# Optimization experiments

Hardware: AMD Instinct MI355X
Metric: run time of the kernel (lower is better)

Reference implementation:

```python
import jax, jax.numpy as jnp
import numpy as np

MAX_ITERS = 10


def setup_inputs() -> dict:
    key = jax.random.key(0)
    k1, k2, k3, k4, k5 = jax.random.split(key, 5)
    B, D, H = 8192, 2048, 2048
    s = 1.0 / np.sqrt(H)  # torch default init scale (uniform); we use scaled normal
    return {
        "encoded": jax.random.normal(k1, (B, D), dtype=jnp.float32),
        "w_ih": jax.random.normal(k2, (3 * H, D), dtype=jnp.float32) * s,
        "w_hh": jax.random.normal(k3, (3 * H, H), dtype=jnp.float32) * s,
        "b_ih": jax.random.normal(k4, (3 * H,), dtype=jnp.float32) * s,
        "b_hh": jax.random.normal(k5, (3 * H,), dtype=jnp.float32) * s,
    }


def reference(encoded, w_ih, w_hh, b_ih, b_hh):
    """Iterative GRUCell recurrence (training-mode: full max_iters, no early exit).

    PyTorch GRUCell math:
      r = sigmoid(W_ir x + b_ir + W_hr h + b_hr)
      z = sigmoid(W_iz x + b_iz + W_hz h + b_hz)
      n = tanh(W_in x + b_in + r * (W_hn h + b_hn))
      h' = (1 - z) * n + z * h
    """
    H = w_hh.shape[1]
    # Input projection is constant across iterations (gru_input never changes).
    gi = encoded @ w_ih.T + b_ih  # [B, 3H]
    gi_r, gi_z, gi_n = gi[:, :H], gi[:, H:2 * H], gi[:, 2 * H:]

    def step(h, _):
        gh = h @ w_hh.T + b_hh  # [B, 3H]
        gh_r, gh_z, gh_n = gh[:, :H], gh[:, H:2 * H], gh[:, 2 * H:]
        r = jax.nn.sigmoid(gi_r + gh_r)
        z = jax.nn.sigmoid(gi_z + gh_z)
        n = jnp.tanh(gi_n + r * gh_n)
        h_next = (1.0 - z) * n + z * h
        return h_next, None

    h0 = jnp.zeros((encoded.shape[0], H), dtype=encoded.dtype)
    h, _ = jax.lax.scan(step, h0, None, length=MAX_ITERS)
    return h
```

## Files before the change

kernel.cpp:

```cpp
#include <hip/hip_runtime.h>

typedef _Float16 f16_t;
typedef _Float16 f16x4 __attribute__((ext_vector_type(4)));
typedef _Float16 f16x8 __attribute__((ext_vector_type(8)));
typedef float floatx4 __attribute__((ext_vector_type(4)));

#define GLDS16(gptr, lptr) __builtin_amdgcn_global_load_lds( \
    (const __attribute__((address_space(1))) void*)(gptr),   \
    (__attribute__((address_space(3))) void*)(lptr), 16, 0, 0)

__device__ __forceinline__ float sigmoidf_fast(float x) {
    return 1.f / (1.f + __expf(-x));
}
__device__ __forceinline__ float tanhf_fast(float x) {
    float e = __expf(2.f * x);
    return 1.f - 2.f / (e + 1.f);
}

#define GATE_STRIDE 16777216L

__global__ __launch_bounds__(256)
void cvt_f32_f16(const float* __restrict__ in, f16_t* __restrict__ out, long n)
{
    long i = ((long)blockIdx.x * 256 + threadIdx.x) * 8;
    if (i >= n) return;
    floatx4 a = *(const floatx4*)(in + i);
    floatx4 b = *(const floatx4*)(in + i + 4);
    f16x8 o;
    o[0] = (f16_t)a[0]; o[1] = (f16_t)a[1]; o[2] = (f16_t)a[2]; o[3] = (f16_t)a[3];
    o[4] = (f16_t)b[0]; o[5] = (f16_t)b[1]; o[6] = (f16_t)b[2]; o[7] = (f16_t)b[3];
    *(f16x8*)(out + i) = o;
}

__global__ __launch_bounds__(256, 2)
void gemm_gi(const f16_t* __restrict__ A,
             const f16_t* __restrict__ W,
             const float* __restrict__ bias,
             f16_t* __restrict__ giF)
{
    const int K = 2048;
    __shared__ __align__(16) f16_t As[128 * 32];
    __shared__ __align__(16) f16_t Ws[128 * 32];
    const int tid  = threadIdx.x;
    const int lane = tid & 63;
    const int wave = tid >> 6;
    const int m0 = blockIdx.x * 128;
    const int n0 = blockIdx.y * 128;
    const int wm = (wave >> 1) * 64;
    const int wn = (wave & 1) * 64;

    floatx4 acc[4][4] = {};

    const int srow = lane >> 2;
    const int skc  = (((lane & 3) ^ ((srow >> 1) & 3))) * 8;
    const int fr = lane & 15;
    const int jq = lane >> 4;
    const int jsw = (jq ^ ((fr >> 1) & 3)) * 8;

    for (int k0 = 0; k0 < K; k0 += 32) {
        #pragma unroll
        for (int j = 0; j < 2; ++j) {
            int c = j * 4 + wave;
            int row = c * 16 + srow;
            GLDS16(A + (size_t)(m0 + row) * K + k0 + skc, As + c * 512);
        }
        #pragma unroll
        for (int j = 0; j < 2; ++j) {
            int c = j * 4 + wave;
            int row = c * 16 + srow;
            GLDS16(W + (size_t)(n0 + row) * K + k0 + skc, Ws + c * 512);
        }
        __syncthreads();

        f16x8 a_frag[4], b_frag[4];
        #pragma unroll
        for (int t = 0; t < 4; ++t)
            a_frag[t] = *(const f16x8*)(As + (wm + t * 16 + fr) * 32 + jsw);
        #pragma unroll
        for (int t = 0; t < 4; ++t)
            b_frag[t] = *(const f16x8*)(Ws + (wn + t * 16 + fr) * 32 + jsw);
        #pragma unroll
        for (int tm = 0; tm < 4; ++tm)
            #pragma unroll
            for (int tn = 0; tn < 4; ++tn)
                acc[tm][tn] = __builtin_amdgcn_mfma_f32_16x16x32_f16(
                    a_frag[tm], b_frag[tn], acc[tm][tn], 0, 0, 0);
        __syncthreads();
    }

    const int g   = n0 >> 11;
    const int tNb = ((n0 & 2047) >> 4) + (wn >> 4);
    #pragma unroll
    for (int tm = 0; tm < 4; ++tm) {
        int tM = (m0 + wm + tm * 16) >> 4;
        #pragma unroll
        for (int tn = 0; tn < 4; ++tn) {
            int tN = tNb + tn;
            int n  = n0 + wn + tn * 16 + fr;
            float b = bias[n];
            f16x4 v;
            #pragma unroll
            for (int r = 0; r < 4; ++r) v[r] = (f16_t)(acc[tm][tn][r] + b);
            *(f16x4*)(giF + ((size_t)(g * 512 + tM) * 128 + tN) * 256 + lane * 4) = v;
        }
    }
}

__global__ __launch_bounds__(256)
void gru_init(const f16_t* __restrict__ giF,
              const float* __restrict__ bhh,
              f16_t* __restrict__ h16)
{
    const int H = 2048;
    __shared__ __align__(16) f16_t hp[128 * 72];
    const int tid  = threadIdx.x;
    const int lane = tid & 63;
    const int wave = tid >> 6;
    const int m0 = blockIdx.x * 128;
    const int n0 = blockIdx.y * 64;
    const int wm = (wave >> 1) * 64;
    const int wn = (wave & 1) * 32;
    const int colL = lane & 15;
    const int rq = (lane >> 4) * 4;

    #pragma unroll
    for (int tm = 0; tm < 4; ++tm) {
        int tM = (m0 + wm + tm * 16) >> 4;
        #pragma unroll
        for (int tn = 0; tn < 2; ++tn) {
            int tN = ((n0 + wn) >> 4) + tn;
            size_t base = ((size_t)tM * 128 + tN) * 256 + lane * 4;
            f16x4 g_r = *(const f16x4*)(giF + base);
            f16x4 g_z = *(const f16x4*)(giF + base + GATE_STRIDE);
            f16x4 g_n = *(const f16x4*)(giF + base + 2 * GATE_STRIDE);
            int n = n0 + wn + tn * 16 + colL;
            float br = bhh[n], bz = bhh[H + n], bn = bhh[2 * H + n];
            #pragma unroll
            for (int r = 0; r < 4; ++r) {
                float rr = sigmoidf_fast((float)g_r[r] + br);
                float zz = sigmoidf_fast((float)g_z[r] + bz);
                float nn = tanhf_fast((float)g_n[r] + rr * bn);
                float h = (1.f - zz) * nn;
                hp[(wm + tm * 16 + rq + r) * 72 + wn + tn * 16 + colL] = (f16_t)h;
            }
        }
    }
    __syncthreads();
    #pragma unroll
    for (int i = 0; i < 4; ++i) {
        int r2 = i * 32 + (tid >> 3);
        int ch = tid & 7;
        f16x8 v = *(const f16x8*)(hp + r2 * 72 + ch * 8);
        *(f16x8*)(h16 + (size_t)(m0 + r2) * H + n0 + ch * 8) = v;
    }
}

__global__ __launch_bounds__(256, 2)
void gru_step(const f16_t* __restrict__ Wh,
              const float* __restrict__ bhh,
              const f16_t* __restrict__ giF,
              const f16_t* __restrict__ hin,
              f16_t* __restrict__ hout,
              float* __restrict__ out32)
{
    const int K = 2048, H = 2048;
    __shared__ __align__(16) f16_t smem[128 * 64 + 3 * 64 * 64];
    f16_t* As  = smem;
    f16_t* Wsm = smem + 128 * 64;
    const int tid  = threadIdx.x;
    const int lane = tid & 63;
    const int wave = tid >> 6;

    const int bid   = blockIdx.x;
    const int xcd   = bid & 7;
    const int rblk  = bid >> 3;
    const int m0 = (rblk >> 2) * 128;
    const int n0 = (xcd * 4 + (rblk & 3)) * 64;

    const int wm = (wave >> 1) * 64;
    const int wn = (wave & 1) * 32;

    floatx4 acc[3][4][2] = {};

    const int srow8 = lane >> 3;
    const int sgk   = ((lane & 7) ^ srow8) * 8;
    const int fr = lane & 15;
    const int jq = lane >> 4;
    const int rq = (lane >> 4) * 4;

    f16x4 hold16[4][2];

    for (int k0 = 0; k0 < K; k0 += 64) {
        #pragma unroll
        for (int j = 0; j < 4; ++j) {
            int c = j * 4 + wave;
            int row = c * 8 + srow8;
            GLDS16(hin + (size_t)(m0 + row) * K + k0 + sgk, As + c * 512);
        }
        #pragma unroll
        for (int j = 0; j < 6; ++j) {
            int c = j * 4 + wave;
            int g = c >> 3;
            int cw = c & 7;
            int row = cw * 8 + srow8;
            GLDS16(Wh + (size_t)(g * H + n0 + row) * K + k0 + sgk,
                   Wsm + c * 512);
        }
        __syncthreads();

        if (k0 == n0) {
            #pragma unroll
            for (int tm = 0; tm < 4; ++tm) {
                #pragma unroll
                for (int tn = 0; tn < 2; ++tn) {
                    #pragma unroll
                    for (int r = 0; r < 4; ++r) {
                        int row_a = wm + tm * 16 + rq + r;
                        int kloc  = wn + tn * 16 + fr;
                        int slot  = (kloc >> 3) ^ (row_a & 7);
                        hold16[tm][tn][r] =
                            As[row_a * 64 + slot * 8 + (kloc & 7)];
                    }
                }
            }
        }

        #pragma unroll
        for (int ksub = 0; ksub < 2; ++ksub) {
            f16x8 a_frag[4];
            #pragma unroll
            for (int t = 0; t < 4; ++t) {
                int row = wm + t * 16 + fr;
                int slot = (ksub * 4 + jq) ^ (row & 7);
                a_frag[t] = *(const f16x8*)(As + row * 64 + slot * 8);
            }
            #pragma unroll
            for (int g = 0; g < 3; ++g) {
                #pragma unroll
                for (int tn = 0; tn < 2; ++tn) {
                    int row_w = wn + tn * 16 + fr;
                    int slot = (ksub * 4 + jq) ^ (row_w & 7);
                    f16x8 b_frag = *(const f16x8*)(Wsm + g * 4096 +
                                                   row_w * 64 + slot * 8);
                    #pragma unroll
                    for (int tm = 0; tm < 4; ++tm)
                        acc[g][tm][tn] = __builtin_amdgcn_mfma_f32_16x16x32_f16(
                            a_frag[tm], b_frag, acc[g][tm][tn], 0, 0, 0);
                }
            }
        }
        __syncthreads();
    }

    f16x4 hv[4][2];
    #pragma unroll
    for (int tm = 0; tm < 4; ++tm) {
        int tM = (m0 + wm + tm * 16) >> 4;
        #pragma unroll
        for (int tn = 0; tn < 2; ++tn) {
            int tN = ((n0 + wn) >> 4) + tn;
            size_t base = ((size_t)tM * 128 + tN) * 256 + lane * 4;
            f16x4 g_r = *(const f16x4*)(giF + base);
            f16x4 g_z = *(const f16x4*)(giF + base + GATE_STRIDE);
            f16x4 g_n = *(const f16x4*)(giF + base + 2 * GATE_STRIDE);
            int n = n0 + wn + tn * 16 + fr;
            float br = bhh[n], bz = bhh[H + n], bn = bhh[2 * H + n];
            #pragma unroll
            for (int r = 0; r < 4; ++r) {
                int m = m0 + wm + tm * 16 + rq + r;
                float rr = sigmoidf_fast((float)g_r[r] + acc[0][tm][tn][r] + br);
                float zz = sigmoidf_fast((float)g_z[r] + acc[1][tm][tn][r] + bz);
                float nn = tanhf_fast((float)g_n[r] +
                                      rr * (acc[2][tm][tn][r] + bn));
                float hold = (float)hold16[tm][tn][r];
                float hnew = (1.f - zz) * nn + zz * hold;
                hv[tm][tn][r] = (f16_t)hnew;
                if (out32) out32[(size_t)m * H + n] = hnew;
            }
        }
    }

    if (!out32) {
        f16_t* hp = smem;
        #pragma unroll
        for (int tm = 0; tm < 4; ++tm)
            #pragma unroll
            for (int tn = 0; tn < 2; ++tn)
                #pragma unroll
                for (int r = 0; r < 4; ++r)
                    hp[(wm + tm * 16 + rq + r) * 72 + wn + tn * 16 + fr] =
                        hv[tm][tn][r];
        __syncthreads();
        #pragma unroll
        for (int i = 0; i < 4; ++i) {
            int r2 = i * 32 + (tid >> 3);
            int ch = tid & 7;
            f16x8 v = *(const f16x8*)(hp + r2 * 72 + ch * 8);
            *(f16x8*)(hout + (size_t)(m0 + r2) * H + n0 + ch * 8) = v;
        }
    }
}

extern "C" void kernel_launch(void* const* d_in, const int* in_sizes, int n_in,
                              void* d_out, int out_size, void* d_ws, size_t ws_size,
                              hipStream_t stream) {
    const float* x    = (const float*)d_in[0];
    const float* w_ih = (const float*)d_in[1];
    const float* w_hh = (const float*)d_in[2];
    const float* b_ih = (const float*)d_in[3];
    const float* b_hh = (const float*)d_in[4];
    float* out = (float*)d_out;

    char* ws = (char*)d_ws;
    f16_t* xh    = (f16_t*)(ws);
    f16_t* wih_h = (f16_t*)(ws + 33554432);
    f16_t* whh_h = (f16_t*)(ws + 33554432 + 25165824);
    f16_t* gi    = (f16_t*)(ws + 33554432 + 2 * 25165824);
    f16_t* h16a  = (f16_t*)(ws + 33554432 + 2 * 25165824 + 100663296);
    f16_t* h16b  = (f16_t*)(ws + 33554432 + 2 * 25165824 + 100663296 + 33554432);

    cvt_f32_f16<<<dim3(8192), 256, 0, stream>>>(x, xh, 16777216L);
    cvt_f32_f16<<<dim3(6144), 256, 0, stream>>>(w_ih, wih_h, 12582912L);
    cvt_f32_f16<<<dim3(6144), 256, 0, stream>>>(w_hh, whh_h, 12582912L);

    gemm_gi<<<dim3(64, 48), 256, 0, stream>>>(xh, wih_h, b_ih, gi);
    gru_init<<<dim3(64, 32), 256, 0, stream>>>(gi, b_hh, h16a);

    f16_t* hin = h16a; f16_t* hout = h16b;
    for (int it = 2; it <= 10; ++it) {
        float* o32 = (it == 10) ? out : nullptr;
        gru_step<<<dim3(2048), 256, 0, stream>>>(whh_h, b_hh, gi,
                                                 hin, hout, o32);
        f16_t* t = hin; hin = hout; hout = t;
    }
}
```

Baseline: 2.525 ms.

## Switch GRU GEMMs to 32x32x16 MFMA and fuse input projection with init step

```diff
diff --git a/kernel.cpp b/kernel.cpp
--- a/kernel.cpp
+++ b/kernel.cpp
@@ -1,9 +1,9 @@
 #include <hip/hip_runtime.h>
 
 typedef _Float16 f16_t;
-typedef _Float16 f16x4 __attribute__((ext_vector_type(4)));
 typedef _Float16 f16x8 __attribute__((ext_vector_type(8)));
 typedef float floatx4 __attribute__((ext_vector_type(4)));
+typedef float floatx16 __attribute__((ext_vector_type(16)));
 
 #define GLDS16(gptr, lptr) __builtin_amdgcn_global_load_lds( \
     (const __attribute__((address_space(1))) void*)(gptr),   \
@@ -17,7 +17,6 @@
     return 1.f - 2.f / (e + 1.f);
 }
 
-#define GATE_STRIDE 16777216L
 
 __global__ __launch_bounds__(256)
 void cvt_f32_f16(const float* __restrict__ in, f16_t* __restrict__ out, long n)
@@ -32,136 +31,13 @@
     *(f16x8*)(out + i) = o;
 }
 
-__global__ __launch_bounds__(256, 2)
-void gemm_gi(const f16_t* __restrict__ A,
-             const f16_t* __restrict__ W,
-             const float* __restrict__ bias,
-             f16_t* __restrict__ giF)
-{
-    const int K = 2048;
-    __shared__ __align__(16) f16_t As[128 * 32];
-    __shared__ __align__(16) f16_t Ws[128 * 32];
-    const int tid  = threadIdx.x;
-    const int lane = tid & 63;
-    const int wave = tid >> 6;
-    const int m0 = blockIdx.x * 128;
-    const int n0 = blockIdx.y * 128;
-    const int wm = (wave >> 1) * 64;
-    const int wn = (wave & 1) * 64;
-
-    floatx4 acc[4][4] = {};
-
-    const int srow = lane >> 2;
-    const int skc  = (((lane & 3) ^ ((srow >> 1) & 3))) * 8;
-    const int fr = lane & 15;
-    const int jq = lane >> 4;
-    const int jsw = (jq ^ ((fr >> 1) & 3)) * 8;
-
-    for (int k0 = 0; k0 < K; k0 += 32) {
-        #pragma unroll
-        for (int j = 0; j < 2; ++j) {
-            int c = j * 4 + wave;
-            int row = c * 16 + srow;
-            GLDS16(A + (size_t)(m0 + row) * K + k0 + skc, As + c * 512);
-        }
-        #pragma unroll
-        for (int j = 0; j < 2; ++j) {
-            int c = j * 4 + wave;
-            int row = c * 16 + srow;
-            GLDS16(W + (size_t)(n0 + row) * K + k0 + skc, Ws + c * 512);
-        }
-        __syncthreads();
-
-        f16x8 a_frag[4], b_frag[4];
-        #pragma unroll
-        for (int t = 0; t < 4; ++t)
-            a_frag[t] = *(const f16x8*)(As + (wm + t * 16 + fr) * 32 + jsw);
-        #pragma unroll
-        for (int t = 0; t < 4; ++t)
-            b_frag[t] = *(const f16x8*)(Ws + (wn + t * 16 + fr) * 32 + jsw);
-        #pragma unroll
-        for (int tm = 0; tm < 4; ++tm)
-            #pragma unroll
-            for (int tn = 0; tn < 4; ++tn)
-                acc[tm][tn] = __builtin_amdgcn_mfma_f32_16x16x32_f16(
-                    a_frag[tm], b_frag[tn], acc[tm][tn], 0, 0, 0);
-        __syncthreads();
-    }
-
-    const int g   = n0 >> 11;
-    const int tNb = ((n0 & 2047) >> 4) + (wn >> 4);
-    #pragma unroll
-    for (int tm = 0; tm < 4; ++tm) {
-        int tM = (m0 + wm + tm * 16) >> 4;
-        #pragma unroll
-        for (int tn = 0; tn < 4; ++tn) {
-            int tN = tNb + tn;
-            int n  = n0 + wn + tn * 16 + fr;
-            float b = bias[n];
-            f16x4 v;
-            #pragma unroll
-            for (int r = 0; r < 4; ++r) v[r] = (f16_t)(acc[tm][tn][r] + b);
-            *(f16x4*)(giF + ((size_t)(g * 512 + tM) * 128 + tN) * 256 + lane * 4) = v;
-        }
-    }
-}
-
-__global__ __launch_bounds__(256)
-void gru_init(const f16_t* __restrict__ giF,
-              const float* __restrict__ bhh,
-              f16_t* __restrict__ h16)
-{
-    const int H = 2048;
-    __shared__ __align__(16) f16_t hp[128 * 72];
-    const int tid  = threadIdx.x;
-    const int lane = tid & 63;
-    const int wave = tid >> 6;
-    const int m0 = blockIdx.x * 128;
-    const int n0 = blockIdx.y * 64;
-    const int wm = (wave >> 1) * 64;
-    const int wn = (wave & 1) * 32;
-    const int colL = lane & 15;
-    const int rq = (lane >> 4) * 4;
-
-    #pragma unroll
-    for (int tm = 0; tm < 4; ++tm) {
-        int tM = (m0 + wm + tm * 16) >> 4;
-        #pragma unroll
-        for (int tn = 0; tn < 2; ++tn) {
-            int tN = ((n0 + wn) >> 4) + tn;
-            size_t base = ((size_t)tM * 128 + tN) * 256 + lane * 4;
-            f16x4 g_r = *(const f16x4*)(giF + base);
-            f16x4 g_z = *(const f16x4*)(giF + base + GATE_STRIDE);
-            f16x4 g_n = *(const f16x4*)(giF + base + 2 * GATE_STRIDE);
-            int n = n0 + wn + tn * 16 + colL;
-            float br = bhh[n], bz = bhh[H + n], bn = bhh[2 * H + n];
-            #pragma unroll
-            for (int r = 0; r < 4; ++r) {
-                float rr = sigmoidf_fast((float)g_r[r] + br);
-                float zz = sigmoidf_fast((float)g_z[r] + bz);
-                float nn = tanhf_fast((float)g_n[r] + rr * bn);
-                float h = (1.f - zz) * nn;
-                hp[(wm + tm * 16 + rq + r) * 72 + wn + tn * 16 + colL] = (f16_t)h;
-            }
-        }
-    }
-    __syncthreads();
-    #pragma unroll
-    for (int i = 0; i < 4; ++i) {
-        int r2 = i * 32 + (tid >> 3);
-        int ch = tid & 7;
-        f16x8 v = *(const f16x8*)(hp + r2 * 72 + ch * 8);
-        *(f16x8*)(h16 + (size_t)(m0 + r2) * H + n0 + ch * 8) = v;
-    }
-}
-
-__global__ __launch_bounds__(256, 2)
-void gru_step(const f16_t* __restrict__ Wh,
-              const float* __restrict__ bhh,
-              const f16_t* __restrict__ giF,
-              const f16_t* __restrict__ hin,
-              f16_t* __restrict__ hout,
-              float* __restrict__ out32)
+__global__ __launch_bounds__(256, 3)
+void gemm_gi32(const f16_t* __restrict__ Xh,
+               const f16_t* __restrict__ Wih,
+               const float* __restrict__ bih,
+               const float* __restrict__ bhh,
+               f16_t* __restrict__ giF,
+               f16_t* __restrict__ h16out)
 {
     const int K = 2048, H = 2048;
     __shared__ __align__(16) f16_t smem[128 * 64 + 3 * 64 * 64];
@@ -171,24 +47,144 @@
     const int lane = tid & 63;
     const int wave = tid >> 6;
 
-    const int bid   = blockIdx.x;
-    const int xcd   = bid & 7;
-    const int rblk  = bid >> 3;
+    const int bid  = blockIdx.x;
+    const int xcd  = bid & 7;
+    const int rblk = bid >> 3;
     const int m0 = (rblk >> 2) * 128;
     const int n0 = (xcd * 4 + (rblk & 3)) * 64;
 
     const int wm = (wave >> 1) * 64;
     const int wn = (wave & 1) * 32;
 
-    floatx4 acc[3][4][2] = {};
+    floatx16 acc[3][2] = {};
 
     const int srow8 = lane >> 3;
     const int sgk   = ((lane & 7) ^ srow8) * 8;
-    const int fr = lane & 15;
-    const int jq = lane >> 4;
-    const int rq = (lane >> 4) * 4;
-
-    f16x4 hold16[4][2];
+    const int c31   = lane & 31;
+    const int half  = lane >> 5;
+
+    for (int k0 = 0; k0 < K; k0 += 64) {
+        #pragma unroll
+        for (int j = 0; j < 4; ++j) {
+            int c = j * 4 + wave;
+            int row = c * 8 + srow8;
+            GLDS16(Xh + (size_t)(m0 + row) * K + k0 + sgk, As + c * 512);
+        }
+        #pragma unroll
+        for (int j = 0; j < 6; ++j) {
+            int c = j * 4 + wave;
+            int g = c >> 3;
+            int cw = c & 7;
+            int row = cw * 8 + srow8;
+            GLDS16(Wih + (size_t)(g * H + n0 + row) * K + k0 + sgk,
+                   Wsm + c * 512);
+        }
+        __syncthreads();
+
+        #pragma unroll
+        for (int ksub = 0; ksub < 4; ++ksub) {
+            int gk = ksub * 2 + half;
+            f16x8 a_frag[2];
+            #pragma unroll
+            for (int tm = 0; tm < 2; ++tm) {
+                int row = wm + tm * 32 + c31;
+                int slot = gk ^ (row & 7);
+                a_frag[tm] = *(const f16x8*)(As + row * 64 + slot * 8);
+            }
+            #pragma unroll
+            for (int g = 0; g < 3; ++g) {
+                int row_w = wn + c31;
+                int slot = gk ^ (row_w & 7);
+                f16x8 b_frag = *(const f16x8*)(Wsm + g * 4096 +
+                                               row_w * 64 + slot * 8);
+                #pragma unroll
+                for (int tm = 0; tm < 2; ++tm)
+                    acc[g][tm] = __builtin_amdgcn_mfma_f32_32x32x16_f16(
+                        a_frag[tm], b_frag, acc[g][tm], 0, 0, 0);
+            }
+        }
+        __syncthreads();
+    }
+
+    const int n   = n0 + wn + c31;
+    const int tN  = (n0 + wn) >> 5;
+    const int rhi = half * 4;
+    const float br = bhh[n], bz = bhh[H + n], bnn = bhh[2 * H + n];
+    const float bir = bih[n], biz = bih[H + n], bin = bih[2 * H + n];
+    f16_t* hp = smem;
+    #pragma unroll
+    for (int tm = 0; tm < 2; ++tm) {
+        int tM = (m0 + wm + tm * 32) >> 5;
+        f16x8 s[3][2];
+        #pragma unroll
+        for (int r = 0; r < 16; ++r) {
+            float gr = acc[0][tm][r] + bir;
+            float gz = acc[1][tm][r] + biz;
+            float gn = acc[2][tm][r] + bin;
+            if (r < 8) {
+                s[0][0][r] = (f16_t)gr; s[1][0][r] = (f16_t)gz; s[2][0][r] = (f16_t)gn;
+            } else {
+                s[0][1][r-8] = (f16_t)gr; s[1][1][r-8] = (f16_t)gz; s[2][1][r-8] = (f16_t)gn;
+            }
+            float rr = sigmoidf_fast(gr + br);
+            float zz = sigmoidf_fast(gz + bz);
+            float nn = tanhf_fast(gn + rr * bnn);
+            float h = (1.f - zz) * nn;
+            int ml = wm + tm * 32 + (r & 3) + 8 * (r >> 2) + rhi;
+            hp[ml * 72 + wn + c31] = (f16_t)h;
+        }
+        #pragma unroll
+        for (int g = 0; g < 3; ++g) {
+            size_t off = ((size_t)(g * 256 + tM) * 64 + tN) * 1024 + lane * 16;
+            *(f16x8*)(giF + off)     = s[g][0];
+            *(f16x8*)(giF + off + 8) = s[g][1];
+        }
+    }
+    __syncthreads();
+    #pragma unroll
+    for (int i = 0; i < 4; ++i) {
+        int r2 = i * 32 + (tid >> 3);
+        int ch = tid & 7;
+        f16x8 v = *(const f16x8*)(hp + r2 * 72 + ch * 8);
+        *(f16x8*)(h16out + (size_t)(m0 + r2) * H + n0 + ch * 8) = v;
+    }
+}
+
+__global__ __launch_bounds__(256, 3)
+void gru_step32(const f16_t* __restrict__ Wh,
+                const float* __restrict__ bhh,
+                const f16_t* __restrict__ giF,
+                const f16_t* __restrict__ hin,
+                f16_t* __restrict__ hout,
+                float* __restrict__ out32)
+{
+    const int K = 2048, H = 2048;
+    __shared__ __align__(16) f16_t smem[128 * 64 + 3 * 64 * 64];
+    f16_t* As  = smem;
+    f16_t* Wsm = smem + 128 * 64;
+    const int tid  = threadIdx.x;
+    const int lane = tid & 63;
+    const int wave = tid >> 6;
+
+    const int bid  = blockIdx.x;
+    const int xcd  = bid & 7;
+    const int rblk = bid >> 3;
+    const int m0 = (rblk >> 2) * 128;
+    const int n0 = (xcd * 4 + (rblk & 3)) * 64;
+
+    const int wm = (wave >> 1) * 64;
+    const int wn = (wave & 1) * 32;
+
+    floatx16 acc[3][2] = {};
+
+    const int srow8 = lane >> 3;
+    const int sgk   = ((lane & 7) ^ srow8) * 8;
+    const int c31   = lane & 31;
+    const int half  = lane >> 5;
+    const int rhi   = half * 4;
+    const int kloc  = wn + c31;
+
+    f16_t hold[2][16];
 
     for (int k0 = 0; k0 < K; k0 += 64) {
         #pragma unroll
@@ -210,87 +206,79 @@
 
         if (k0 == n0) {
             #pragma unroll
-            for (int tm = 0; tm < 4; ++tm) {
+            for (int tm = 0; tm < 2; ++tm)
                 #pragma unroll
-                for (int tn = 0; tn < 2; ++tn) {
-                    #pragma unroll
-                    for (int r = 0; r < 4; ++r) {
-                        int row_a = wm + tm * 16 + rq + r;
-                        int kloc  = wn + tn * 16 + fr;
-                        int slot  = (kloc >> 3) ^ (row_a & 7);
-                        hold16[tm][tn][r] =
-                            As[row_a * 64 + slot * 8 + (kloc & 7)];
-                    }
+                for (int r = 0; r < 16; ++r) {
+                    int ml = wm + tm * 32 + (r & 3) + 8 * (r >> 2) + rhi;
+                    int slot = (kloc >> 3) ^ (ml & 7);
+                    hold[tm][r] = As[ml * 64 + slot * 8 + (kloc & 7)];
                 }
-            }
-        }
-
-        #pragma unroll
-        for (int ksub = 0; ksub < 2; ++ksub) {
-            f16x8 a_frag[4];
-            #pragma unroll
-            for (int t = 0; t < 4; ++t) {
-                int row = wm + t * 16 + fr;
-                int slot = (ksub * 4 + jq) ^ (row & 7);
-                a_frag[t] = *(const f16x8*)(As + row * 64 + slot * 8);
+        }
+
+        #pragma unroll
+        for (int ksub = 0; ksub < 4; ++ksub) {
+            int gk = ksub * 2 + half;
+            f16x8 a_frag[2];
+            #pragma unroll
+            for (int tm = 0; tm < 2; ++tm) {
+                int row = wm + tm * 32 + c31;
+                int slot = gk ^ (row & 7);
+                a_frag[tm] = *(const f16x8*)(As + row * 64 + slot * 8);
             }
             #pragma unroll
             for (int g = 0; g < 3; ++g) {
+                int row_w = wn + c31;
+                int slot = gk ^ (row_w & 7);
+                f16x8 b_frag = *(const f16x8*)(Wsm + g * 4096 +
+                                               row_w * 64 + slot * 8);
                 #pragma unroll
-                for (int tn = 0; tn < 2; ++tn) {
-                    int row_w = wn + tn * 16 + fr;
-                    int slot = (ksub * 4 + jq) ^ (row_w & 7);
-                    f16x8 b_frag = *(const f16x8*)(Wsm + g * 4096 +
-                                                   row_w * 64 + slot * 8);
-                    #pragma unroll
-                    for (int tm = 0; tm < 4; ++tm)
-                        acc[g][tm][tn] = __builtin_amdgcn_mfma_f32_16x16x32_f16(
-                            a_frag[tm], b_frag, acc[g][tm][tn], 0, 0, 0);
-                }
+                for (int tm = 0; tm < 2; ++tm)
+                    acc[g][tm] = __builtin_amdgcn_mfma_f32_32x32x16_f16(
+                        a_frag[tm], b_frag, acc[g][tm], 0, 0, 0);
             }
         }
         __syncthreads();
     }
 
-    f16x4 hv[4][2];
+    const int n  = n0 + wn + c31;
+    const int tN = (n0 + wn) >> 5;
+    const float br = bhh[n], bz = bhh[H + n], bnn = bhh[2 * H + n];
+    f16_t* hp   = smem;
+    float* hp32 = (float*)smem;
     #pragma unroll
-    for (int tm = 0; tm < 4; ++tm) {
-        int tM = (m0 + wm + tm * 16) >> 4;
-        #pragma unroll
-        for (int tn = 0; tn < 2; ++tn) {
-            int tN = ((n0 + wn) >> 4) + tn;
-            size_t base = ((size_t)tM * 128 + tN) * 256 + lane * 4;
-            f16x4 g_r = *(const f16x4*)(giF + base);
-            f16x4 g_z = *(const f16x4*)(giF + base + GATE_STRIDE);
-            f16x4 g_n = *(const f16x4*)(giF + base + 2 * GATE_STRIDE);
-            int n = n0 + wn + tn * 16 + fr;
-            float br = bhh[n], bz = bhh[H + n], bn = bhh[2 * H + n];
-            #pragma unroll
-            for (int r = 0; r < 4; ++r) {
-                int m = m0 + wm + tm * 16 + rq + r;
-                float rr = sigmoidf_fast((float)g_r[r] + acc[0][tm][tn][r] + br);
-                float zz = sigmoidf_fast((float)g_z[r] + acc[1][tm][tn][r] + bz);
-                float nn = tanhf_fast((float)g_n[r] +
-                                      rr * (acc[2][tm][tn][r] + bn));
-                float hold = (float)hold16[tm][tn][r];
-                float hnew = (1.f - zz) * nn + zz * hold;
-                hv[tm][tn][r] = (f16_t)hnew;
-                if (out32) out32[(size_t)m * H + n] = hnew;
-            }
-        }
-    }
-
-    if (!out32) {
-        f16_t* hp = smem;
-        #pragma unroll
-        for (int tm = 0; tm < 4; ++tm)
-            #pragma unroll
-            for (int tn = 0; tn < 2; ++tn)
-                #pragma unroll
-                for (int r = 0; r < 4; ++r)
-                    hp[(wm + tm * 16 + rq + r) * 72 + wn + tn * 16 + fr] =
-                        hv[tm][tn][r];
-        __syncthreads();
+    for (int tm = 0; tm < 2; ++tm) {
+        int tM = (m0 + wm + tm * 32) >> 5;
+        f16x8 glo[3], ghi[3];
+        #pragma unroll
+        for (int g = 0; g < 3; ++g) {
+            size_t off = ((size_t)(g * 256 + tM) * 64 + tN) * 1024 + lane * 16;
+            glo[g] = *(const f16x8*)(giF + off);
+            ghi[g] = *(const f16x8*)(giF + off + 8);
+        }
+        #pragma unroll
+        for (int r = 0; r < 16; ++r) {
+            float gir = (float)((r < 8) ? glo[0][r] : ghi[0][r - 8]);
+            float giz = (float)((r < 8) ? glo[1][r] : ghi[1][r - 8]);
+            float gin = (float)((r < 8) ? glo[2][r] : ghi[2][r - 8]);
+            float rr = sigmoidf_fast(gir + acc[0][tm][r] + br);
+            float zz = sigmoidf_fast(giz + acc[1][tm][r] + bz);
+            float nn = tanhf_fast(gin + rr * (acc[2][tm][r] + bnn));
+            float hnew = (1.f - zz) * nn + zz * (float)hold[tm][r];
+            int ml = wm + tm * 32 + (r & 3) + 8 * (r >> 2) + rhi;
+            if (out32) hp32[ml * 68 + wn + c31] = hnew;
+            else       hp[ml * 72 + wn + c31]   = (f16_t)hnew;
+        }
+    }
+    __syncthreads();
+    if (out32) {
+        #pragma unroll
+        for (int i = 0; i < 8; ++i) {
+            int r2 = i * 16 + (tid >> 4);
+            int c4 = (tid & 15) * 4;
+            floatx4 v = *(const floatx4*)(hp32 + r2 * 68 + c4);
+            *(floatx4*)(out32 + (size_t)(m0 + r2) * H + n0 + c4) = v;
+        }
+    } else {
         #pragma unroll
         for (int i = 0; i < 4; ++i) {
             int r2 = i * 32 + (tid >> 3);
@@ -323,14 +311,13 @@
     cvt_f32_f16<<<dim3(6144), 256, 0, stream>>>(w_ih, wih_h, 12582912L);
     cvt_f32_f16<<<dim3(6144), 256, 0, stream>>>(w_hh, whh_h, 12582912L);
 
-    gemm_gi<<<dim3(64, 48), 256, 0, stream>>>(xh, wih_h, b_ih, gi);
-    gru_init<<<dim3(64, 32), 256, 0, stream>>>(gi, b_hh, h16a);
+    gemm_gi32<<<dim3(2048), 256, 0, stream>>>(xh, wih_h, b_ih, b_hh, gi, h16a);
 
     f16_t* hin = h16a; f16_t* hout = h16b;
     for (int it = 2; it <= 10; ++it) {
         float* o32 = (it == 10) ? out : nullptr;
-        gru_step<<<dim3(2048), 256, 0, stream>>>(whh_h, b_hh, gi,
-                                                 hin, hout, o32);
+        gru_step32<<<dim3(2048), 256, 0, stream>>>(whh_h, b_hh, gi,
+                                                   hin, hout, o32);
         f16_t* t = hin; hin = hout; hout = t;
     }
 }
```

New measurement: 2.993 ms. +18.5%, slower.
